# Kernel optimization log

Measured on AMD Instinct MI355X. Metric: run time of the kernel, lower is better.

## Reference

```python
import jax, jax.numpy as jnp
import numpy as np

EPS = 1e-5  # torch InstanceNorm1d default eps


def _instance_norm(x, gamma, beta):
    # per-sample, per-channel stats over the length dim; biased variance (torch semantics)
    mu = jnp.mean(x, axis=-1, keepdims=True)
    var = jnp.var(x, axis=-1, keepdims=True)
    return (x - mu) / jnp.sqrt(var + EPS) * gamma[None, :, None] + beta[None, :, None]


def _forward(x_ft, gamma, beta):
    # x_ft: complex [B, C, N]
    N = x_ft.shape[-1]
    x = jnp.real(jnp.fft.ifft(x_ft, norm='forward'))  # [B, C, N] real
    # The torch loop runs res = base_res .. N, each iteration overwriting the
    # low/high frequency bands of x_out in-place. The final iteration
    # (res == N) writes EVERY entry of x_out (the two band slices cover all
    # N//2+1 rfft bins), so the module's output -- and its gradients, since
    # overwritten writes carry zero cotangent -- equal the res == N
    # computation alone. resample_1d(x, N) copies the full spectrum and is a
    # spectral identity, so x_res == x.
    xr = _instance_norm(x, gamma, beta)
    xr = jax.nn.gelu(xr, approximate=False)  # exact GELU, matches torch nn.GELU
    # Faithful to the source: inside the loop torch.fft.rfft2 is used, i.e. a
    # 2D transform over the last two dims (channel, length).
    x_out = jnp.fft.rfft2(xr, norm='forward')  # complex [B, C, N//2 + 1]
    out = jnp.fft.fft(jnp.fft.irfft(x_out, n=N, norm='forward'), norm='forward')
    return out  # complex [B, C, N]


def setup_inputs() -> dict:
    key = jax.random.key(0)
    k1, k2 = jax.random.split(key)
    B, C, N = 16, 128, 8192
    return {
        'x_ft_real': jax.random.normal(k1, (B, C, N), dtype=jnp.float32),
        'x_ft_imag': jax.random.normal(k2, (B, C, N), dtype=jnp.float32),
        'gamma': jnp.ones((C,), dtype=jnp.float32),
        'beta': jnp.zeros((C,), dtype=jnp.float32),
    }


def reference(x_ft_real, x_ft_imag, gamma, beta):
    out = _forward(jax.lax.complex(x_ft_real, x_ft_imag), gamma, beta)
    # return real/imag parts as separate float arrays (harness-friendly)
    return (jnp.real(out), jnp.imag(out))
```

## Files before the change

### kernel.cpp

```cpp
#include <hip/hip_runtime.h>
#include <math.h>

static constexpr int kN = 8192;
static constexpr int kC = 128;
static constexpr int kB = 16;
static constexpr float kScale = 0.5f / 1048576.0f;
static constexpr double kTwoPi = 6.28318530717958647692;

#define C8 0.70710678118654752f

__device__ __forceinline__ float2 cadd(float2 a, float2 b){ return make_float2(a.x+b.x, a.y+b.y); }
__device__ __forceinline__ float2 csub(float2 a, float2 b){ return make_float2(a.x-b.x, a.y-b.y); }
__device__ __forceinline__ float2 cmul(float2 a, float2 b){ return make_float2(a.x*b.x-a.y*b.y, a.x*b.y+a.y*b.x); }
__device__ __forceinline__ float2 cconj(float2 a){ return make_float2(a.x, -a.y); }

__device__ __forceinline__ int swz(int n){ return n ^ ((n>>4)&7) ^ (((n>>6)&7)<<3); }

__device__ __forceinline__ float2 W2048(const float2* T, int m){
    float2 tt = T[m & 1023];
    return (m & 1024) ? make_float2(-tt.y, tt.x) : tt;
}

template<int SGN>
__device__ __forceinline__ void dft8(float2* a){
    float2 s0=cadd(a[0],a[4]), s1=csub(a[0],a[4]);
    float2 s2=cadd(a[2],a[6]), s3=csub(a[2],a[6]);
    float2 E0=cadd(s0,s2), E2=csub(s0,s2);
    float2 j3 = (SGN>0)? make_float2(-s3.y, s3.x) : make_float2(s3.y, -s3.x);
    float2 E1=cadd(s1,j3), E3=csub(s1,j3);
    float2 t0=cadd(a[1],a[5]), t1=csub(a[1],a[5]);
    float2 t2=cadd(a[3],a[7]), t3=csub(a[3],a[7]);
    float2 O0=cadd(t0,t2), O2=csub(t0,t2);
    float2 k3 = (SGN>0)? make_float2(-t3.y, t3.x) : make_float2(t3.y, -t3.x);
    float2 O1=cadd(t1,k3), O3=csub(t1,k3);
    float2 W1 = (SGN>0)? make_float2(C8*(O1.x-O1.y), C8*(O1.x+O1.y))
                       : make_float2(C8*(O1.x+O1.y), C8*(O1.y-O1.x));
    float2 W2 = (SGN>0)? make_float2(-O2.y, O2.x) : make_float2(O2.y, -O2.x);
    float2 W3 = (SGN>0)? make_float2(C8*(-O3.x-O3.y), C8*(O3.x-O3.y))
                       : make_float2(C8*(O3.y-O3.x), C8*(-O3.x-O3.y));
    a[0]=cadd(E0,O0); a[4]=csub(E0,O0);
    a[1]=cadd(E1,W1); a[5]=csub(E1,W1);
    a[2]=cadd(E2,W2); a[6]=csub(E2,W2);
    a[3]=cadd(E3,W3); a[7]=csub(E3,W3);
}

__device__ __forceinline__ void twid_apply2(float2* a, float2* b, float2 w1){
    float2 w2=cmul(w1,w1);
    float2 w3=cmul(w2,w1), w4=cmul(w2,w2);
    float2 w5=cmul(w2,w3), w6=cmul(w3,w3), w7=cmul(w3,w4);
    a[1]=cmul(a[1],w1); a[2]=cmul(a[2],w2); a[3]=cmul(a[3],w3);
    a[4]=cmul(a[4],w4); a[5]=cmul(a[5],w5); a[6]=cmul(a[6],w6); a[7]=cmul(a[7],w7);
    b[1]=cmul(b[1],w1); b[2]=cmul(b[2],w2); b[3]=cmul(b[3],w3);
    b[4]=cmul(b[4],w4); b[5]=cmul(b[5],w5); b[6]=cmul(b[6],w6); b[7]=cmul(b[7],w7);
}

__device__ __forceinline__ float gelu_fast(float v){
    float z = v*(0.7978845608028654f + 0.0356774081363001f*v*v);
    float e = __builtin_amdgcn_exp2f(-2.8853900817779268f * z);
    return v / (1.0f + e);
}

__global__ __launch_bounds__(512, 4) void k1_row(
    const float* __restrict__ xr, const float* __restrict__ xi,
    const float* __restrict__ gamma, const float* __restrict__ beta,
    float* __restrict__ outR, float* __restrict__ outI)
{
    __shared__ float4 buf[4096];
    __shared__ float2 T[1024];

    const int t    = threadIdx.x;
    const int row0 = blockIdx.x * 2;

    for (int i = t; i < 1024; i += 512) {
        float s, c;
        sincosf((float)(kTwoPi/4096.0 * (double)i), &s, &c);
        T[i] = make_float2(c, s);
    }
    __syncthreads();

    const float2 E = make_float2(0.9999997058628822f, 7.669903187427045e-4f);
    const int l   = t & 63;
    const int s64 = ((t>>6)*512 + l) ^ (l>>4);
    const int u = t & 7, G = t >> 3, g = G & 7;
    const int s8 = (G<<6) + (g<<3) + (u ^ ((G&1)<<2));
    const int s1 = (t<<3) ^ ((t>>1)&7) ^ (((t>>3)&7)<<3);
    const int s0 = swz(t);

    float2 v0[8], v1[8];

    const float* r0R = xr + (size_t)row0 * kN;
    const float* r0I = xi + (size_t)row0 * kN;
    const float* r1R = r0R + kN;
    const float* r1I = r0I + kN;

    #pragma unroll
    for (int j = 0; j < 8; ++j) {
        int k   = t + (j<<9);
        int km  = (kN - k) & (kN-1);
        int km2 = 4096 - k;
        float2 w = W2048(T, k>>1);
        if (t & 1) w = cmul(w, E);
        {
            float2 Hk  = make_float2(r0R[k]+r0R[km],       r0I[k]-r0I[km]);
            float2 Hk2 = make_float2(r0R[k+4096]+r0R[km2], r0I[k+4096]-r0I[km2]);
            float2 S = cadd(Hk,Hk2), D = csub(Hk,Hk2);
            float2 P = cmul(D, w);
            v0[j] = make_float2(S.x - P.y, S.y + P.x);
        }
        {
            float2 Hk  = make_float2(r1R[k]+r1R[km],       r1I[k]-r1I[km]);
            float2 Hk2 = make_float2(r1R[k+4096]+r1R[km2], r1I[k+4096]-r1I[km2]);
            float2 S = cadd(Hk,Hk2), D = csub(Hk,Hk2);
            float2 P = cmul(D, w);
            v1[j] = make_float2(S.x - P.y, S.y + P.x);
        }
    }
    dft8<1>(v0); dft8<1>(v1);
    twid_apply2(v0, v1, T[t]);
    #pragma unroll
    for (int j = 0; j < 8; ++j)
        buf[s0 + (j<<9)] = make_float4(v0[j].x, v0[j].y, v1[j].x, v1[j].y);
    __syncthreads();

    #pragma unroll
    for (int j = 0; j < 8; ++j) {
        float4 p = buf[s64 ^ ((j<<6)|(j<<3)|((j&1)<<2))];
        v0[j] = make_float2(p.x, p.y); v1[j] = make_float2(p.z, p.w);
    }
    dft8<1>(v0); dft8<1>(v1);
    twid_apply2(v0, v1, T[l<<3]);
    #pragma unroll
    for (int j = 0; j < 8; ++j)
        buf[s64 ^ ((j<<6)|(j<<3)|((j&1)<<2))] = make_float4(v0[j].x, v0[j].y, v1[j].x, v1[j].y);
    __syncthreads();

    #pragma unroll
    for (int j = 0; j < 8; ++j) {
        float4 p = buf[s8 ^ ((j<<3)|(j>>1))];
        v0[j] = make_float2(p.x, p.y); v1[j] = make_float2(p.z, p.w);
    }
    dft8<1>(v0); dft8<1>(v1);
    twid_apply2(v0, v1, T[u<<6]);
    #pragma unroll
    for (int j = 0; j < 8; ++j)
        buf[s8 ^ ((j<<3)|(j>>1))] = make_float4(v0[j].x, v0[j].y, v1[j].x, v1[j].y);
    __syncthreads();

    #pragma unroll
    for (int j = 0; j < 8; ++j) {
        float4 p = buf[s1 ^ j];
        v0[j] = make_float2(p.x, p.y); v1[j] = make_float2(p.z, p.w);
    }
    dft8<1>(v0); dft8<1>(v1);

    float ps0 = 0.f, pq0 = 0.f, ps1 = 0.f, pq1 = 0.f;
    #pragma unroll
    for (int j = 0; j < 8; ++j) {
        ps0 += v0[j].x + v0[j].y;  pq0 += v0[j].x*v0[j].x + v0[j].y*v0[j].y;
        ps1 += v1[j].x + v1[j].y;  pq1 += v1[j].x*v1[j].x + v1[j].y*v1[j].y;
    }
    #pragma unroll
    for (int off = 32; off >= 1; off >>= 1) {
        ps0 += __shfl_down(ps0, off);  pq0 += __shfl_down(pq0, off);
        ps1 += __shfl_down(ps1, off);  pq1 += __shfl_down(pq1, off);
    }
    if ((t & 63) == 0) buf[(t>>6)<<9] = make_float4(ps0, pq0, ps1, pq1);
    __syncthreads();
    float sum0=0.f, sq0=0.f, sum1=0.f, sq1=0.f;
    #pragma unroll
    for (int w = 0; w < 8; ++w) {
        float4 p = buf[w<<9];
        sum0 += p.x; sq0 += p.y; sum1 += p.z; sq1 += p.w;
    }
    __syncthreads();
    {
        float mean = sum0 * (1.0f/8192.0f);
        float var  = sq0  * (1.0f/8192.0f) - mean*mean;
        float gg = gamma[row0 & (kC-1)] * rsqrtf(var + 1e-5f);
        float bb = beta[row0 & (kC-1)] - mean * gg;
        #pragma unroll
        for (int j = 0; j < 8; ++j) {
            v0[j].x = gelu_fast(v0[j].x * gg + bb);
            v0[j].y = gelu_fast(v0[j].y * gg + bb);
        }
    }
    {
        float mean = sum1 * (1.0f/8192.0f);
        float var  = sq1  * (1.0f/8192.0f) - mean*mean;
        float gg = gamma[(row0+1) & (kC-1)] * rsqrtf(var + 1e-5f);
        float bb = beta[(row0+1) & (kC-1)] - mean * gg;
        #pragma unroll
        for (int j = 0; j < 8; ++j) {
            v1[j].x = gelu_fast(v1[j].x * gg + bb);
            v1[j].y = gelu_fast(v1[j].y * gg + bb);
        }
    }

    dft8<-1>(v0); dft8<-1>(v1);
    #pragma unroll
    for (int j = 0; j < 8; ++j)
        buf[s1 ^ j] = make_float4(v0[j].x, v0[j].y, v1[j].x, v1[j].y);
    __syncthreads();

    #pragma unroll
    for (int j = 0; j < 8; ++j) {
        float4 p = buf[s8 ^ ((j<<3)|(j>>1))];
        v0[j] = make_float2(p.x, p.y); v1[j] = make_float2(p.z, p.w);
    }
    twid_apply2(v0, v1, cconj(T[u<<6]));
    dft8<-1>(v0); dft8<-1>(v1);
    #pragma unroll
    for (int j = 0; j < 8; ++j)
        buf[s8 ^ ((j<<3)|(j>>1))] = make_float4(v0[j].x, v0[j].y, v1[j].x, v1[j].y);
    __syncthreads();

    #pragma unroll
    for (int j = 0; j < 8; ++j) {
        float4 p = buf[s64 ^ ((j<<6)|(j<<3)|((j&1)<<2))];
        v0[j] = make_float2(p.x, p.y); v1[j] = make_float2(p.z, p.w);
    }
    twid_apply2(v0, v1, cconj(T[l<<3]));
    dft8<-1>(v0); dft8<-1>(v1);
    #pragma unroll
    for (int j = 0; j < 8; ++j)
        buf[s64 ^ ((j<<6)|(j<<3)|((j&1)<<2))] = make_float4(v0[j].x, v0[j].y, v1[j].x, v1[j].y);
    __syncthreads();

    #pragma unroll
    for (int j = 0; j < 8; ++j) {
        float4 p = buf[s0 + (j<<9)];
        v0[j] = make_float2(p.x, p.y); v1[j] = make_float2(p.z, p.w);
    }
    twid_apply2(v0, v1, cconj(T[t]));
    dft8<-1>(v0); dft8<-1>(v1);
    #pragma unroll
    for (int j = 0; j < 8; ++j)
        buf[s0 + (j<<9)] = make_float4(v0[j].x, v0[j].y, v1[j].x, v1[j].y);
    __syncthreads();

    float* o0R = outR + (size_t)row0 * kN;
    float* o0I = outI + (size_t)row0 * kN;
    float* o1R = o0R + kN;
    float* o1I = o0I + kN;
    #pragma unroll
    for (int j = 0; j < 8; ++j) {
        int k = t + (j<<9);
        float4 pm = buf[swz((4096 - k) & 4095)];
        float2 w = W2048(T, k>>1);
        if (t & 1) w = cmul(w, E);
        w = cconj(w);
        {
            float2 Z = v0[j], Zm = make_float2(pm.x, pm.y);
            float2 S = make_float2(Z.x+Zm.x, Z.y-Zm.y);
            float2 D = make_float2(Z.x-Zm.x, Z.y+Zm.y);
            float2 P = cmul(D, w);
            o0R[k] = S.x + P.y;
            o0I[k] = S.y - P.x;
        }
        {
            float2 Z = v1[j], Zm = make_float2(pm.z, pm.w);
            float2 S = make_float2(Z.x+Zm.x, Z.y-Zm.y);
            float2 D = make_float2(Z.x-Zm.x, Z.y+Zm.y);
            float2 P = cmul(D, w);
            o1R[k] = S.x + P.y;
            o1I[k] = S.y - P.x;
        }
    }
    if (t == 0) {
        o0R[4096] = 2.0f*(v0[0].x - v0[0].y);
        o0I[4096] = 0.f;
        o1R[4096] = 2.0f*(v1[0].x - v1[0].y);
        o1I[4096] = 0.f;
    }
}

__global__ __launch_bounds__(256,4) void k2_col(float* __restrict__ outR,
                                                float* __restrict__ outI)
{
    __shared__ float2 tile[kC][32];
    __shared__ float2 tw[64];

    const int tid = threadIdx.x;
    const int k   = tid & 31;
    const int g   = tid >> 5;
    const int b   = blockIdx.y;
    const int kk  = (blockIdx.x << 5) + k;
    const bool valid = (kk <= 4096);

    if (tid < 64) {
        float s, c;
        sincosf((float)(kTwoPi/128.0 * (double)tid), &s, &c);
        tw[tid] = make_float2(c, -s);
    }
    float* baseR = outR + (size_t)b * kC * kN;
    float* baseI = outI + (size_t)b * kC * kN;
    for (int c = g; c < kC; c += 8) {
        size_t off = (size_t)c * kN + kk;
        tile[c][k] = valid ? make_float2(baseR[off], baseI[off])
                           : make_float2(0.f, 0.f);
    }
    __syncthreads();

    for (int st = 7; st >= 1; --st) {
        const int h = 1 << (st-1);
        #pragma unroll
        for (int s = 0; s < 8; ++s) {
            int q   = g + (s<<3);
            int pos = q & (h-1);
            int i0  = ((q >> (st-1)) << st) + pos;
            int i1  = i0 + h;
            float2 a = tile[i0][k], bb = tile[i1][k];
            float2 w = tw[pos << (7-st)];
            tile[i0][k] = cadd(a, bb);
            tile[i1][k] = cmul(csub(a, bb), w);
        }
        __syncthreads();
    }

    if (valid) {
        for (int p = g; p < kC; p += 8) {
            int f = (int)(__brev((unsigned)p) >> 25);
            float2 v = tile[p][k];
            v.x *= kScale; v.y *= kScale;
            size_t off = (size_t)f * kN + kk;
            if (kk == 0 || kk == 4096) {
                baseR[off] = v.x; baseI[off] = 0.f;
            } else {
                baseR[off] = v.x; baseI[off] = v.y;
                size_t offm = (size_t)f * kN + (kN - kk);
                baseR[offm] = v.x; baseI[offm] = -v.y;
            }
        }
    }
}

extern "C" void kernel_launch(void* const* d_in, const int* in_sizes, int n_in,
                              void* d_out, int out_size, void* d_ws, size_t ws_size,
                              hipStream_t stream)
{
    const float* xr    = (const float*)d_in[0];
    const float* xi    = (const float*)d_in[1];
    const float* gamma = (const float*)d_in[2];
    const float* beta  = (const float*)d_in[3];

    float* outR = (float*)d_out;
    float* outI = outR + (size_t)kB * kC * kN;

    k1_row<<<kB * kC / 2, 512, 0, stream>>>(xr, xi, gamma, beta, outR, outI);
    k2_col<<<dim3(129, kB), 256, 0, stream>>>(outR, outI);
}
```

Baseline: 122.7 us.

## Move real-FFT post-processing into column kernel and relax intra-wave barriers

The final real-spectrum split (pairing bin k with bin N-k and applying twiddles) moves out of the row kernel into the column kernel. The row kernel now stores the raw half-size FFT output directly, with no final LDS round trip. The column kernel handles paired columns k and 4096-k together, cutting its grid roughly in half, and computes per-column twiddles with sincosf. Several block-wide barriers in the row kernel become wave barriers where the data exchange is assumed to stay within one wavefront, and the reduction moves to a small dedicated shared array so one sync can be dropped. This risks races if those exchange stages actually cross waves, and it raises LDS use and lowers occupancy in the column kernel.

```diff
diff --git a/kernel.cpp b/kernel.cpp
--- a/kernel.cpp
+++ b/kernel.cpp
@@ -67,6 +67,7 @@
 {
     __shared__ float4 buf[4096];
     __shared__ float2 T[1024];
+    __shared__ float4 sred[8];
 
     const int t    = threadIdx.x;
     const int row0 = blockIdx.x * 2;
@@ -132,7 +133,7 @@
     #pragma unroll
     for (int j = 0; j < 8; ++j)
         buf[s64 ^ ((j<<6)|(j<<3)|((j&1)<<2))] = make_float4(v0[j].x, v0[j].y, v1[j].x, v1[j].y);
-    __syncthreads();
+    __builtin_amdgcn_wave_barrier();
 
     #pragma unroll
     for (int j = 0; j < 8; ++j) {
@@ -144,7 +145,7 @@
     #pragma unroll
     for (int j = 0; j < 8; ++j)
         buf[s8 ^ ((j<<3)|(j>>1))] = make_float4(v0[j].x, v0[j].y, v1[j].x, v1[j].y);
-    __syncthreads();
+    __builtin_amdgcn_wave_barrier();
 
     #pragma unroll
     for (int j = 0; j < 8; ++j) {
@@ -164,15 +165,14 @@
         ps0 += __shfl_down(ps0, off);  pq0 += __shfl_down(pq0, off);
         ps1 += __shfl_down(ps1, off);  pq1 += __shfl_down(pq1, off);
     }
-    if ((t & 63) == 0) buf[(t>>6)<<9] = make_float4(ps0, pq0, ps1, pq1);
+    if ((t & 63) == 0) sred[t>>6] = make_float4(ps0, pq0, ps1, pq1);
     __syncthreads();
     float sum0=0.f, sq0=0.f, sum1=0.f, sq1=0.f;
     #pragma unroll
     for (int w = 0; w < 8; ++w) {
-        float4 p = buf[w<<9];
+        float4 p = sred[w];
         sum0 += p.x; sq0 += p.y; sum1 += p.z; sq1 += p.w;
     }
-    __syncthreads();
     {
         float mean = sum0 * (1.0f/8192.0f);
         float var  = sq0  * (1.0f/8192.0f) - mean*mean;
@@ -200,7 +200,7 @@
     #pragma unroll
     for (int j = 0; j < 8; ++j)
         buf[s1 ^ j] = make_float4(v0[j].x, v0[j].y, v1[j].x, v1[j].y);
-    __syncthreads();
+    __builtin_amdgcn_wave_barrier();
 
     #pragma unroll
     for (int j = 0; j < 8; ++j) {
@@ -212,7 +212,7 @@
     #pragma unroll
     for (int j = 0; j < 8; ++j)
         buf[s8 ^ ((j<<3)|(j>>1))] = make_float4(v0[j].x, v0[j].y, v1[j].x, v1[j].y);
-    __syncthreads();
+    __builtin_amdgcn_wave_barrier();
 
     #pragma unroll
     for (int j = 0; j < 8; ++j) {
@@ -233,10 +233,6 @@
     }
     twid_apply2(v0, v1, cconj(T[t]));
     dft8<-1>(v0); dft8<-1>(v1);
-    #pragma unroll
-    for (int j = 0; j < 8; ++j)
-        buf[s0 + (j<<9)] = make_float4(v0[j].x, v0[j].y, v1[j].x, v1[j].y);
-    __syncthreads();
 
     float* o0R = outR + (size_t)row0 * kN;
     float* o0I = outI + (size_t)row0 * kN;
@@ -245,82 +241,80 @@
     #pragma unroll
     for (int j = 0; j < 8; ++j) {
         int k = t + (j<<9);
-        float4 pm = buf[swz((4096 - k) & 4095)];
-        float2 w = W2048(T, k>>1);
-        if (t & 1) w = cmul(w, E);
-        w = cconj(w);
-        {
-            float2 Z = v0[j], Zm = make_float2(pm.x, pm.y);
-            float2 S = make_float2(Z.x+Zm.x, Z.y-Zm.y);
-            float2 D = make_float2(Z.x-Zm.x, Z.y+Zm.y);
-            float2 P = cmul(D, w);
-            o0R[k] = S.x + P.y;
-            o0I[k] = S.y - P.x;
-        }
-        {
-            float2 Z = v1[j], Zm = make_float2(pm.z, pm.w);
-            float2 S = make_float2(Z.x+Zm.x, Z.y-Zm.y);
-            float2 D = make_float2(Z.x-Zm.x, Z.y+Zm.y);
-            float2 P = cmul(D, w);
-            o1R[k] = S.x + P.y;
-            o1I[k] = S.y - P.x;
-        }
-    }
-    if (t == 0) {
-        o0R[4096] = 2.0f*(v0[0].x - v0[0].y);
-        o0I[4096] = 0.f;
-        o1R[4096] = 2.0f*(v1[0].x - v1[0].y);
-        o1I[4096] = 0.f;
-    }
-}
-
-__global__ __launch_bounds__(256,4) void k2_col(float* __restrict__ outR,
-                                                float* __restrict__ outI)
+        o0R[k] = v0[j].x;  o0I[k] = v0[j].y;
+        o1R[k] = v1[j].x;  o1I[k] = v1[j].y;
+    }
+}
+
+__global__ __launch_bounds__(256, 2) void k2_col(float* __restrict__ outR,
+                                                 float* __restrict__ outI)
 {
-    __shared__ float2 tile[kC][32];
+    __shared__ float2 tile[kC][64];
     __shared__ float2 tw[64];
 
-    const int tid = threadIdx.x;
-    const int k   = tid & 31;
-    const int g   = tid >> 5;
-    const int b   = blockIdx.y;
-    const int kk  = (blockIdx.x << 5) + k;
-    const bool valid = (kk <= 4096);
+    const int tid  = threadIdx.x;
+    const int b    = blockIdx.y;
+    const int k0   = blockIdx.x << 5;
+    const int j    = tid & 31;
+    const int g    = tid >> 5;
+    const int colA = k0 + j;
+    const bool valid = (colA <= 2048);
+    const int colB = (4096 - colA) & 4095;
 
     if (tid < 64) {
         float s, c;
         sincosf((float)(kTwoPi/128.0 * (double)tid), &s, &c);
         tw[tid] = make_float2(c, -s);
     }
+
+    float ws, wc;
+    sincosf((float)(-kTwoPi/8192.0 * (double)colA), &ws, &wc);
+
     float* baseR = outR + (size_t)b * kC * kN;
     float* baseI = outI + (size_t)b * kC * kN;
+
     for (int c = g; c < kC; c += 8) {
-        size_t off = (size_t)c * kN + kk;
-        tile[c][k] = valid ? make_float2(baseR[off], baseI[off])
-                           : make_float2(0.f, 0.f);
-    }
-    __syncthreads();
-
+        float2 YA = make_float2(0.f, 0.f), YB = make_float2(0.f, 0.f);
+        if (valid) {
+            size_t offA = (size_t)c * kN + colA;
+            size_t offB = (size_t)c * kN + colB;
+            float Zx  = baseR[offA], Zy  = baseI[offA];
+            float Zmx = baseR[offB], Zmy = baseI[offB];
+            float Sx = Zx + Zmx, Sy = Zy - Zmy;
+            float Dx = Zx - Zmx, Dy = Zy + Zmy;
+            float Px = Dx*wc - Dy*ws, Py = Dx*ws + Dy*wc;
+            YA = make_float2(Sx + Py,  Sy - Px);
+            YB = make_float2(Sx - Py, -Sy - Px);
+        }
+        tile[c][j]      = YA;
+        tile[c][j + 32] = YB;
+    }
+    __syncthreads();
+
+    const int kc = tid & 63;
+    const int gg = tid >> 6;
     for (int st = 7; st >= 1; --st) {
         const int h = 1 << (st-1);
         #pragma unroll
-        for (int s = 0; s < 8; ++s) {
-            int q   = g + (s<<3);
+        for (int s = 0; s < 16; ++s) {
+            int q   = gg + (s<<2);
             int pos = q & (h-1);
             int i0  = ((q >> (st-1)) << st) + pos;
             int i1  = i0 + h;
-            float2 a = tile[i0][k], bb = tile[i1][k];
+            float2 a = tile[i0][kc], bb = tile[i1][kc];
             float2 w = tw[pos << (7-st)];
-            tile[i0][k] = cadd(a, bb);
-            tile[i1][k] = cmul(csub(a, bb), w);
+            tile[i0][kc] = cadd(a, bb);
+            tile[i1][kc] = cmul(csub(a, bb), w);
         }
         __syncthreads();
     }
 
-    if (valid) {
-        for (int p = g; p < kC; p += 8) {
+    const int cA = (kc < 32) ? (k0 + kc) : (k0 + kc - 32);
+    const int kk = (kc < 32) ? cA : (4096 - cA);
+    if (cA <= 2048) {
+        for (int p = gg; p < kC; p += 4) {
             int f = (int)(__brev((unsigned)p) >> 25);
-            float2 v = tile[p][k];
+            float2 v = tile[p][kc];
             v.x *= kScale; v.y *= kScale;
             size_t off = (size_t)f * kN + kk;
             if (kk == 0 || kk == 4096) {
@@ -347,5 +341,5 @@
     float* outI = outR + (size_t)kB * kC * kN;
 
     k1_row<<<kB * kC / 2, 512, 0, stream>>>(xr, xi, gamma, beta, outR, outI);
-    k2_col<<<dim3(129, kB), 256, 0, stream>>>(outR, outI);
-}
+    k2_col<<<dim3(65, kB), 256, 0, stream>>>(outR, outI);
+}
```

After: 153.9 us. 25.4% more time.
